# Kernel optimization log

Measured on AMD Instinct MI355X. Metric: run time of the kernel, lower is better.

The kernel has to match this reference:

```python
import jax, jax.numpy as jnp
import numpy as np

GS = 7          # grid size
NB = 2          # boxes per cell
NC = 20         # classes
LAMBDA_COORD = 0.5
LAMBDA_NOOBJ = 0.5


def setup_inputs() -> dict:
    key = jax.random.key(0)
    k1, k2, k3 = jax.random.split(key, 3)
    B = 8192
    C = 5 * NB + NC  # 30
    inputs = jax.random.uniform(k1, (B, GS, GS, C), minval=0.05, maxval=0.95, dtype=jnp.float32)
    targets = jax.random.uniform(k2, (B, GS, GS, C), minval=0.05, maxval=0.95, dtype=jnp.float32)
    obj = jax.random.bernoulli(k3, 0.15, (B, GS, GS)).astype(jnp.float32)
    # _transform_targets writes the SAME box into both box slots and sets conf=1 for obj cells
    targets = targets.at[..., 5:9].set(targets[..., 0:4])
    targets = targets.at[..., 4].set(obj)
    targets = targets.at[..., 9].set(obj)
    return {"inputs": inputs, "targets": targets}


def _yolo_loss(inputs, targets):
    bs = inputs.shape[0]
    gs = inputs.shape[2]
    dt = inputs.dtype

    conf_t = targets[..., 4]
    coord = (conf_t > 0).astype(dt)          # [B,S,S] cells containing an object
    noobj = (conf_t == 0).astype(dt)          # [B,S,S]

    # ---- no-object confidence loss: channels 4 + 5*b for each box b ----
    conf_idx = jnp.arange(NB) * 5 + 4         # [4, 9]
    pc = inputs[..., conf_idx]                # [B,S,S,NB]
    tc = targets[..., conf_idx]
    loss_noobj = jnp.sum(noobj[..., None] * (pc - tc) ** 2)

    # ---- per-cell box matching (vectorizes the pairwise IoU loop) ----
    bp = inputs[..., :5 * NB].reshape(inputs.shape[:3] + (NB, 5))    # [B,S,S,NB,5]
    # original takes boxes_targets[i] (first box of the pair; both slots are identical)
    bt = targets[..., :5 * NB].reshape(targets.shape[:3] + (NB, 5))[..., 0, :]  # [B,S,S,5]

    def to_xyxy(b):
        # faithful to original: xy scaled by 1/gs, wh NOT scaled
        xy = b[..., :2] / gs
        wh = b[..., 2:4]
        return jnp.concatenate([xy - 0.5 * wh, xy + 0.5 * wh], axis=-1)

    pxy = to_xyxy(bp)                          # [B,S,S,NB,4]
    txy = to_xyxy(bt)[..., None, :]            # [B,S,S,1,4]
    lt = jnp.maximum(pxy[..., :2], txy[..., :2])
    rb = jnp.minimum(pxy[..., 2:], txy[..., 2:])
    whi = jnp.clip(rb - lt, 0.0)
    inter = whi[..., 0] * whi[..., 1]          # [B,S,S,NB]
    area = lambda x: (x[..., 2] - x[..., 0]) * (x[..., 3] - x[..., 1])
    iou = inter / (area(pxy) + area(txy) - inter)   # [B,S,S,NB]

    max_iou = jnp.max(iou, axis=-1)            # [B,S,S]
    idx = jnp.argmax(iou, axis=-1)             # [B,S,S] responsible box (first max, like torch)
    idx_b = jnp.broadcast_to(idx[..., None, None], idx.shape + (1, 5))
    rp = jnp.take_along_axis(bp, idx_b, axis=-2)[..., 0, :]  # [B,S,S,5] responsible preds

    loss_xy = jnp.sum(coord[..., None] * (rp[..., :2] - bt[..., :2]) ** 2)
    loss_wh = jnp.sum(coord[..., None] * (jnp.sqrt(rp[..., 2:4]) - jnp.sqrt(bt[..., 2:4])) ** 2)
    loss_obj = jnp.sum(coord * (rp[..., 4] - max_iou) ** 2)
    loss_class = jnp.sum(coord[..., None] * (inputs[..., 5 * NB:] - targets[..., 5 * NB:]) ** 2)

    loss_boxes = LAMBDA_COORD * (loss_xy + loss_wh) / bs
    loss_conf = (loss_obj + LAMBDA_NOOBJ * loss_noobj) / bs
    loss_class = loss_class / bs
    return loss_boxes, loss_conf, loss_class


def reference(inputs, targets):
    return _yolo_loss(inputs, targets)
```

## Files before the change

### kernel.cpp

```cpp
#include <hip/hip_runtime.h>

#define CC 30
#define TPW 64
#define WPB 4
#define TILE_FLOATS (TPW * CC)
#define TILE_VEC4   (TILE_FLOATS / 4)

#define AS1 __attribute__((address_space(1)))
#define AS3 __attribute__((address_space(3)))

__device__ __forceinline__ void dma16(const float4* gsrc_lane, float4* lds_base) {
    __builtin_amdgcn_global_load_lds((const AS1 unsigned int*)gsrc_lane,
                                     (AS3 unsigned int*)lds_base, 16, 0, 0);
}

__device__ __forceinline__ void prefetch_tile(const float* __restrict__ in,
                                              const float* __restrict__ tg,
                                              int t, float* lin, float* ltg, int lane) {
    const float4* gin = (const float4*)(in + (size_t)t * TILE_FLOATS);
    const float4* gtg = (const float4*)(tg + (size_t)t * TILE_FLOATS);
    float4* vin = (float4*)lin;
    float4* vtg = (float4*)ltg;
    #pragma unroll
    for (int k = 0; k < 7; ++k) {
        dma16(gin + k * 64 + lane, vin + k * 64);
        dma16(gtg + k * 64 + lane, vtg + k * 64);
    }
    if (lane < 32) {
        dma16(gin + 448 + lane, vin + 448);
        dma16(gtg + 448 + lane, vtg + 448);
    }
}

__device__ __forceinline__ void compute_tile(const float* __restrict__ lin,
                                             const float* __restrict__ ltg,
                                             int lane, float inv_gs,
                                             float& a_boxes, float& a_conf, float& a_class) {
    const float2* f2 = (const float2*)(lin + lane * CC);
    const float2* t2 = (const float2*)(ltg + lane * CC);

    const float2 fi0 = f2[0], fi1 = f2[1], fi2 = f2[2], fi3 = f2[3], fi4 = f2[4];
    const float2 tt0 = t2[0], tt1 = t2[1], tt2 = t2[2], tt4 = t2[4];

    const float conf_t = tt2.x;
    const float coord  = (conf_t > 0.0f)  ? 1.0f : 0.0f;
    const float noobj  = (conf_t == 0.0f) ? 1.0f : 0.0f;

    const float d0 = fi2.x - tt2.x;
    const float d1 = fi4.y - tt4.y;
    const float l_noobj = noobj * (d0 * d0 + d1 * d1);

    const float bt0 = tt0.x, bt1 = tt0.y, bt2 = tt1.x, bt3 = tt1.y;
    const float ttx = bt0 * inv_gs, tty = bt1 * inv_gs;
    const float txmin = ttx - 0.5f * bt2, tymin = tty - 0.5f * bt3;
    const float txmax = ttx + 0.5f * bt2, tymax = tty + 0.5f * bt3;
    const float tarea = (txmax - txmin) * (tymax - tymin);

    const float px0 = fi0.x, py0 = fi0.y, pw0 = fi1.x, ph0 = fi1.y, pc0 = fi2.x;
    const float px1 = fi2.y, py1 = fi3.x, pw1 = fi3.y, ph1 = fi4.x, pc1 = fi4.y;

    float iou0, iou1;
    {
        const float cx = px0 * inv_gs, cy = py0 * inv_gs;
        const float xmin = cx - 0.5f * pw0, ymin = cy - 0.5f * ph0;
        const float xmax = cx + 0.5f * pw0, ymax = cy + 0.5f * ph0;
        const float wx = fmaxf(fminf(xmax, txmax) - fmaxf(xmin, txmin), 0.0f);
        const float wy = fmaxf(fminf(ymax, tymax) - fmaxf(ymin, tymin), 0.0f);
        const float inter = wx * wy;
        const float parea = (xmax - xmin) * (ymax - ymin);
        iou0 = inter / (parea + tarea - inter);
    }
    {
        const float cx = px1 * inv_gs, cy = py1 * inv_gs;
        const float xmin = cx - 0.5f * pw1, ymin = cy - 0.5f * ph1;
        const float xmax = cx + 0.5f * pw1, ymax = cy + 0.5f * ph1;
        const float wx = fmaxf(fminf(xmax, txmax) - fmaxf(xmin, txmin), 0.0f);
        const float wy = fmaxf(fminf(ymax, tymax) - fmaxf(ymin, tymin), 0.0f);
        const float inter = wx * wy;
        const float parea = (xmax - xmin) * (ymax - ymin);
        iou1 = inter / (parea + tarea - inter);
    }
    const bool  sel1    = iou1 > iou0;
    const float max_iou = fmaxf(iou0, iou1);

    const float rp0 = sel1 ? px1 : px0;
    const float rp1 = sel1 ? py1 : py0;
    const float rp2 = sel1 ? pw1 : pw0;
    const float rp3 = sel1 ? ph1 : ph0;
    const float rp4 = sel1 ? pc1 : pc0;

    const float dx = rp0 - bt0, dy = rp1 - bt1;
    const float sw = sqrtf(rp2) - sqrtf(bt2);
    const float sh = sqrtf(rp3) - sqrtf(bt3);
    const float dob = rp4 - max_iou;
    const float l_box = dx * dx + dy * dy + sw * sw + sh * sh;
    const float l_obj = dob * dob;

    float l_cls = 0.0f;
    #pragma unroll
    for (int j = 5; j < 15; ++j) {
        const float2 fv = f2[j];
        const float2 tv = t2[j];
        const float gx = fv.x - tv.x;
        const float gy = fv.y - tv.y;
        l_cls += gx * gx + gy * gy;
    }

    a_boxes += coord * l_box;
    a_conf  += coord * l_obj + 0.5f * l_noobj;
    a_class += coord * l_cls;
}

__device__ __forceinline__ void cell_losses_global(const float* __restrict__ f,
                                                   const float* __restrict__ t,
                                                   float& o_boxes, float& o_conf, float& o_cls) {
    const float inv_gs = 0.14285714285714285f;
    const float conf_t = t[4];
    const float coord  = (conf_t > 0.0f)  ? 1.0f : 0.0f;
    const float noobj  = (conf_t == 0.0f) ? 1.0f : 0.0f;
    const float d0 = f[4] - t[4];
    const float d1 = f[9] - t[9];
    const float l_noobj = noobj * (d0 * d0 + d1 * d1);
    const float bt0 = t[0], bt1 = t[1], bt2 = t[2], bt3 = t[3];
    const float ttx = bt0 * inv_gs, tty = bt1 * inv_gs;
    const float txmin = ttx - 0.5f * bt2, tymin = tty - 0.5f * bt3;
    const float txmax = ttx + 0.5f * bt2, tymax = tty + 0.5f * bt3;
    const float tarea = (txmax - txmin) * (tymax - tymin);
    float iou0, iou1;
    {
        const float cx = f[0] * inv_gs, cy = f[1] * inv_gs;
        const float xmin = cx - 0.5f * f[2], ymin = cy - 0.5f * f[3];
        const float xmax = cx + 0.5f * f[2], ymax = cy + 0.5f * f[3];
        const float wx = fmaxf(fminf(xmax, txmax) - fmaxf(xmin, txmin), 0.0f);
        const float wy = fmaxf(fminf(ymax, tymax) - fmaxf(ymin, tymin), 0.0f);
        const float inter = wx * wy;
        const float parea = (xmax - xmin) * (ymax - ymin);
        iou0 = inter / (parea + tarea - inter);
    }
    {
        const float cx = f[5] * inv_gs, cy = f[6] * inv_gs;
        const float xmin = cx - 0.5f * f[7], ymin = cy - 0.5f * f[8];
        const float xmax = cx + 0.5f * f[7], ymax = cy + 0.5f * f[8];
        const float wx = fmaxf(fminf(xmax, txmax) - fmaxf(xmin, txmin), 0.0f);
        const float wy = fmaxf(fminf(ymax, tymax) - fmaxf(ymin, tymin), 0.0f);
        const float inter = wx * wy;
        const float parea = (xmax - xmin) * (ymax - ymin);
        iou1 = inter / (parea + tarea - inter);
    }
    const bool  sel1    = iou1 > iou0;
    const float max_iou = fmaxf(iou0, iou1);
    const float rp0 = sel1 ? f[5] : f[0];
    const float rp1 = sel1 ? f[6] : f[1];
    const float rp2 = sel1 ? f[7] : f[2];
    const float rp3 = sel1 ? f[8] : f[3];
    const float rp4 = sel1 ? f[9] : f[4];
    const float dx = rp0 - bt0, dy = rp1 - bt1;
    const float sw = sqrtf(rp2) - sqrtf(bt2);
    const float sh = sqrtf(rp3) - sqrtf(bt3);
    const float dob = rp4 - max_iou;
    float l_cls = 0.0f;
    #pragma unroll
    for (int j = 10; j < 30; ++j) {
        const float d = f[j] - t[j];
        l_cls += d * d;
    }
    o_boxes += coord * (dx * dx + dy * dy + sw * sw + sh * sh);
    o_conf  += coord * (dob * dob) + 0.5f * l_noobj;
    o_cls   += coord * l_cls;
}

__global__ __launch_bounds__(256) void yolo_main(
        const float* __restrict__ in,
        const float* __restrict__ tg,
        float* __restrict__ ws,
        int ncells, int nwaves_total, int pstride) {
    __shared__ float s_lds[WPB * 2 * TILE_FLOATS];

    const int tid   = threadIdx.x;
    const int lane  = tid & 63;
    const int wave  = tid >> 6;
    const int gwave = blockIdx.x * WPB + wave;

    float* lin = s_lds + wave * (2 * TILE_FLOATS);
    float* ltg = lin + TILE_FLOATS;

    const int nfull = ncells / TPW;
    const float inv_gs = 0.14285714285714285f;

    float a_boxes = 0.0f, a_conf = 0.0f, a_class = 0.0f;

    for (int t = gwave; t < nfull; t += nwaves_total) {
        asm volatile("s_waitcnt lgkmcnt(0)" ::: "memory");
        __builtin_amdgcn_wave_barrier();
        prefetch_tile(in, tg, t, lin, ltg, lane);
        asm volatile("s_waitcnt vmcnt(0)" ::: "memory");
        __builtin_amdgcn_wave_barrier();
        compute_tile(lin, ltg, lane, inv_gs, a_boxes, a_conf, a_class);
        __builtin_amdgcn_wave_barrier();
    }

    #pragma unroll
    for (int off = 32; off > 0; off >>= 1) {
        a_boxes += __shfl_down(a_boxes, off, 64);
        a_conf  += __shfl_down(a_conf,  off, 64);
        a_class += __shfl_down(a_class, off, 64);
    }
    if (lane == 0) {
        ws[gwave]               = a_boxes;
        ws[gwave + pstride]     = a_conf;
        ws[gwave + 2 * pstride] = a_class;
    }
}

__global__ __launch_bounds__(256) void yolo_finalize(
        const float* __restrict__ in,
        const float* __restrict__ tg,
        const float* __restrict__ ws, float* __restrict__ out,
        int nparts, int pstride, int rem_base, int rem, float inv_bs) {
    float b = 0.0f, c = 0.0f, k = 0.0f;
    for (int i = threadIdx.x; i < nparts; i += 256) {
        b += ws[i];
        c += ws[i + pstride];
        k += ws[i + 2 * pstride];
    }
    if ((int)threadIdx.x < rem) {
        const size_t cell = (size_t)(rem_base + threadIdx.x) * CC;
        cell_losses_global(in + cell, tg + cell, b, c, k);
    }
    #pragma unroll
    for (int off = 32; off > 0; off >>= 1) {
        b += __shfl_down(b, off, 64);
        c += __shfl_down(c, off, 64);
        k += __shfl_down(k, off, 64);
    }
    __shared__ float s_red[4][3];
    const int wave = threadIdx.x >> 6;
    if ((threadIdx.x & 63) == 0) {
        s_red[wave][0] = b;
        s_red[wave][1] = c;
        s_red[wave][2] = k;
    }
    __syncthreads();
    if (threadIdx.x == 0) {
        const float tb = s_red[0][0] + s_red[1][0] + s_red[2][0] + s_red[3][0];
        const float tc = s_red[0][1] + s_red[1][1] + s_red[2][1] + s_red[3][1];
        const float tk = s_red[0][2] + s_red[1][2] + s_red[2][2] + s_red[3][2];
        out[0] = 0.5f * tb * inv_bs;
        out[1] = tc * inv_bs;
        out[2] = tk * inv_bs;
    }
}

extern "C" void kernel_launch(void* const* d_in, const int* in_sizes, int n_in,
                              void* d_out, int out_size, void* d_ws, size_t ws_size,
                              hipStream_t stream) {
    const float* in = (const float*)d_in[0];
    const float* tg = (const float*)d_in[1];
    float* out = (float*)d_out;
    float* ws  = (float*)d_ws;

    const int ncells = in_sizes[0] / CC;
    const int B = ncells / 49;
    const float inv_bs = 1.0f / (float)B;

    const int nblocks = 512;
    const int nwaves  = nblocks * WPB;
    const int pstride = nwaves;
    const int nfull   = ncells / TPW;
    const int rem     = ncells - nfull * TPW;

    yolo_main<<<nblocks, 256, 0, stream>>>(in, tg, ws, ncells, nwaves, pstride);
    yolo_finalize<<<1, 256, 0, stream>>>(in, tg, ws, out, nwaves, pstride,
                                         nfull * TPW, rem, inv_bs);
}
```

Measured before the change: 112.0 us.

## Double-buffer half-tiles in LDS and split each cell across lane pairs

Each wave's 64-cell tile is split into two 32-cell halves held in a double-buffered LDS area, so the DMA for the next half is issued before computing the current one (waitcnt vmcnt(8) instead of vmcnt(0)). Each cell is now handled by two lanes, one per predicted box. The lanes exchange IoU values with a shuffle and each sums half of the class channels. This is meant to overlap global-to-LDS loads with compute and shorten the per-lane dependency chain. In exchange it adds a shuffle per half-tile and more loop-control overhead. The odd `f == t` guard and the fixed vmcnt count are fragile.

```diff
diff --git a/kernel.cpp b/kernel.cpp
--- a/kernel.cpp
+++ b/kernel.cpp
@@ -2,9 +2,10 @@
 
 #define CC 30
 #define TPW 64
+#define HALF 32
 #define WPB 4
-#define TILE_FLOATS (TPW * CC)
-#define TILE_VEC4   (TILE_FLOATS / 4)
+#define HALF_FLOATS (HALF * CC)
+#define HALF_VEC4   (HALF_FLOATS / 4)
 
 #define AS1 __attribute__((address_space(1)))
 #define AS3 __attribute__((address_space(3)))
@@ -14,101 +15,90 @@
                                      (AS3 unsigned int*)lds_base, 16, 0, 0);
 }
 
-__device__ __forceinline__ void prefetch_tile(const float* __restrict__ in,
+__device__ __forceinline__ void prefetch_half(const float* __restrict__ in,
                                               const float* __restrict__ tg,
-                                              int t, float* lin, float* ltg, int lane) {
-    const float4* gin = (const float4*)(in + (size_t)t * TILE_FLOATS);
-    const float4* gtg = (const float4*)(tg + (size_t)t * TILE_FLOATS);
+                                              size_t cell_base,
+                                              float* lin, float* ltg, int lane) {
+    const float4* gin = (const float4*)(in + cell_base * CC);
+    const float4* gtg = (const float4*)(tg + cell_base * CC);
     float4* vin = (float4*)lin;
     float4* vtg = (float4*)ltg;
     #pragma unroll
-    for (int k = 0; k < 7; ++k) {
+    for (int k = 0; k < 3; ++k) {
         dma16(gin + k * 64 + lane, vin + k * 64);
         dma16(gtg + k * 64 + lane, vtg + k * 64);
     }
-    if (lane < 32) {
-        dma16(gin + 448 + lane, vin + 448);
-        dma16(gtg + 448 + lane, vtg + 448);
-    }
-}
-
-__device__ __forceinline__ void compute_tile(const float* __restrict__ lin,
+    if (lane < 48) {
+        dma16(gin + 192 + lane, vin + 192);
+        dma16(gtg + 192 + lane, vtg + 192);
+    }
+}
+
+__device__ __forceinline__ void compute_half(const float* __restrict__ lin,
                                              const float* __restrict__ ltg,
                                              int lane, float inv_gs,
                                              float& a_boxes, float& a_conf, float& a_class) {
-    const float2* f2 = (const float2*)(lin + lane * CC);
-    const float2* t2 = (const float2*)(ltg + lane * CC);
-
-    const float2 fi0 = f2[0], fi1 = f2[1], fi2 = f2[2], fi3 = f2[3], fi4 = f2[4];
-    const float2 tt0 = t2[0], tt1 = t2[1], tt2 = t2[2], tt4 = t2[4];
-
-    const float conf_t = tt2.x;
-    const float coord  = (conf_t > 0.0f)  ? 1.0f : 0.0f;
-    const float noobj  = (conf_t == 0.0f) ? 1.0f : 0.0f;
-
-    const float d0 = fi2.x - tt2.x;
-    const float d1 = fi4.y - tt4.y;
-    const float l_noobj = noobj * (d0 * d0 + d1 * d1);
-
-    const float bt0 = tt0.x, bt1 = tt0.y, bt2 = tt1.x, bt3 = tt1.y;
+    const int c = lane >> 1;
+    const int h = lane & 1;
+    const float* f = lin + c * CC;
+    const float* t = ltg + c * CC;
+
+    const int hb = 5 * h;
+    const float px  = f[hb + 0];
+    const float py  = f[hb + 1];
+    const float pw  = f[hb + 2];
+    const float phh = f[hb + 3];
+    const float pc  = f[hb + 4];
+
+    const float bt0 = t[0], bt1 = t[1], bt2 = t[2], bt3 = t[3];
+    const float conf_t  = t[4];
+    const float tconf_h = f == t ? 0.0f : t[hb + 4];
+    const float coord = (conf_t > 0.0f)  ? 1.0f : 0.0f;
+    const float noobj = (conf_t == 0.0f) ? 1.0f : 0.0f;
+
+    const float dn = pc - tconf_h;
+
     const float ttx = bt0 * inv_gs, tty = bt1 * inv_gs;
     const float txmin = ttx - 0.5f * bt2, tymin = tty - 0.5f * bt3;
     const float txmax = ttx + 0.5f * bt2, tymax = tty + 0.5f * bt3;
     const float tarea = (txmax - txmin) * (tymax - tymin);
 
-    const float px0 = fi0.x, py0 = fi0.y, pw0 = fi1.x, ph0 = fi1.y, pc0 = fi2.x;
-    const float px1 = fi2.y, py1 = fi3.x, pw1 = fi3.y, ph1 = fi4.x, pc1 = fi4.y;
-
-    float iou0, iou1;
-    {
-        const float cx = px0 * inv_gs, cy = py0 * inv_gs;
-        const float xmin = cx - 0.5f * pw0, ymin = cy - 0.5f * ph0;
-        const float xmax = cx + 0.5f * pw0, ymax = cy + 0.5f * ph0;
-        const float wx = fmaxf(fminf(xmax, txmax) - fmaxf(xmin, txmin), 0.0f);
-        const float wy = fmaxf(fminf(ymax, tymax) - fmaxf(ymin, tymin), 0.0f);
-        const float inter = wx * wy;
-        const float parea = (xmax - xmin) * (ymax - ymin);
-        iou0 = inter / (parea + tarea - inter);
-    }
-    {
-        const float cx = px1 * inv_gs, cy = py1 * inv_gs;
-        const float xmin = cx - 0.5f * pw1, ymin = cy - 0.5f * ph1;
-        const float xmax = cx + 0.5f * pw1, ymax = cy + 0.5f * ph1;
-        const float wx = fmaxf(fminf(xmax, txmax) - fmaxf(xmin, txmin), 0.0f);
-        const float wy = fmaxf(fminf(ymax, tymax) - fmaxf(ymin, tymin), 0.0f);
-        const float inter = wx * wy;
-        const float parea = (xmax - xmin) * (ymax - ymin);
-        iou1 = inter / (parea + tarea - inter);
-    }
-    const bool  sel1    = iou1 > iou0;
+    const float cx = px * inv_gs, cy = py * inv_gs;
+    const float xmin = cx - 0.5f * pw, ymin = cy - 0.5f * phh;
+    const float xmax = cx + 0.5f * pw, ymax = cy + 0.5f * phh;
+    const float wx = fmaxf(fminf(xmax, txmax) - fmaxf(xmin, txmin), 0.0f);
+    const float wy = fmaxf(fminf(ymax, tymax) - fmaxf(ymin, tymin), 0.0f);
+    const float inter = wx * wy;
+    const float parea = (xmax - xmin) * (ymax - ymin);
+    const float iou_mine = inter / (parea + tarea - inter);
+
+    const float iou_other = __shfl_xor(iou_mine, 1, 64);
+    const float iou0 = h ? iou_other : iou_mine;
+    const float iou1 = h ? iou_mine  : iou_other;
+    const bool  sel1 = iou1 > iou0;
     const float max_iou = fmaxf(iou0, iou1);
-
-    const float rp0 = sel1 ? px1 : px0;
-    const float rp1 = sel1 ? py1 : py0;
-    const float rp2 = sel1 ? pw1 : pw0;
-    const float rp3 = sel1 ? ph1 : ph0;
-    const float rp4 = sel1 ? pc1 : pc0;
-
-    const float dx = rp0 - bt0, dy = rp1 - bt1;
-    const float sw = sqrtf(rp2) - sqrtf(bt2);
-    const float sh = sqrtf(rp3) - sqrtf(bt3);
-    const float dob = rp4 - max_iou;
-    const float l_box = dx * dx + dy * dy + sw * sw + sh * sh;
-    const float l_obj = dob * dob;
-
-    float l_cls = 0.0f;
-    #pragma unroll
-    for (int j = 5; j < 15; ++j) {
-        const float2 fv = f2[j];
-        const float2 tv = t2[j];
+    const float own = ((h == 1) == sel1) ? 1.0f : 0.0f;
+
+    const float dx = px - bt0, dy = py - bt1;
+    const float sw = sqrtf(pw)  - sqrtf(bt2);
+    const float sh = sqrtf(phh) - sqrtf(bt3);
+    const float dob = pc - max_iou;
+
+    a_boxes += own * coord * (dx * dx + dy * dy + sw * sw + sh * sh);
+    a_conf  += own * coord * (dob * dob) + 0.5f * noobj * dn * dn;
+
+    const float2* f2 = (const float2*)f;
+    const float2* t2 = (const float2*)t;
+    float l = 0.0f;
+    #pragma unroll
+    for (int j = 0; j < 5; ++j) {
+        const float2 fv = f2[5 + 5 * h + j];
+        const float2 tv = t2[5 + 5 * h + j];
         const float gx = fv.x - tv.x;
         const float gy = fv.y - tv.y;
-        l_cls += gx * gx + gy * gy;
-    }
-
-    a_boxes += coord * l_box;
-    a_conf  += coord * l_obj + 0.5f * l_noobj;
-    a_class += coord * l_cls;
+        l += gx * gx + gy * gy;
+    }
+    a_class += coord * l;
 }
 
 __device__ __forceinline__ void cell_losses_global(const float* __restrict__ f,
@@ -174,29 +164,47 @@
         const float* __restrict__ tg,
         float* __restrict__ ws,
         int ncells, int nwaves_total, int pstride) {
-    __shared__ float s_lds[WPB * 2 * TILE_FLOATS];
+    __shared__ float s_lds[WPB * 2 * 2 * HALF_FLOATS];
 
     const int tid   = threadIdx.x;
     const int lane  = tid & 63;
     const int wave  = tid >> 6;
     const int gwave = blockIdx.x * WPB + wave;
 
-    float* lin = s_lds + wave * (2 * TILE_FLOATS);
-    float* ltg = lin + TILE_FLOATS;
+    float* base = s_lds + wave * (2 * 2 * HALF_FLOATS);
+    float* bin[2] = { base,                    base + 2 * HALF_FLOATS };
+    float* btg[2] = { base + HALF_FLOATS,      base + 3 * HALF_FLOATS };
 
     const int nfull = ncells / TPW;
     const float inv_gs = 0.14285714285714285f;
 
     float a_boxes = 0.0f, a_conf = 0.0f, a_class = 0.0f;
 
-    for (int t = gwave; t < nfull; t += nwaves_total) {
-        asm volatile("s_waitcnt lgkmcnt(0)" ::: "memory");
-        __builtin_amdgcn_wave_barrier();
-        prefetch_tile(in, tg, t, lin, ltg, lane);
-        asm volatile("s_waitcnt vmcnt(0)" ::: "memory");
-        __builtin_amdgcn_wave_barrier();
-        compute_tile(lin, ltg, lane, inv_gs, a_boxes, a_conf, a_class);
-        __builtin_amdgcn_wave_barrier();
+    int ct = gwave;
+    if (ct < nfull) {
+        prefetch_half(in, tg, (size_t)ct * TPW, bin[0], btg[0], lane);
+        int chalf = 0;
+        int cur = 0;
+        while (true) {
+            int nt = ct, nh = chalf + 1;
+            if (nh == 2) { nh = 0; nt = ct + nwaves_total; }
+            const bool has_next = (nt < nfull);
+
+            asm volatile("s_waitcnt lgkmcnt(0)" ::: "memory");
+            __builtin_amdgcn_wave_barrier();
+            if (has_next)
+                prefetch_half(in, tg, (size_t)nt * TPW + (size_t)nh * HALF,
+                              bin[cur ^ 1], btg[cur ^ 1], lane);
+            __builtin_amdgcn_wave_barrier();
+            if (has_next) asm volatile("s_waitcnt vmcnt(8)" ::: "memory");
+            else          asm volatile("s_waitcnt vmcnt(0)" ::: "memory");
+            __builtin_amdgcn_wave_barrier();
+            compute_half(bin[cur], btg[cur], lane, inv_gs, a_boxes, a_conf, a_class);
+            __builtin_amdgcn_wave_barrier();
+
+            if (!has_next) break;
+            ct = nt; chalf = nh; cur ^= 1;
+        }
     }
 
     #pragma unroll
```

New measurement: 115.5 us. +3.1%, slower.
